# Kernel tuning notes

Hardware: AMD Instinct MI355X
Metric: run time of the kernel (lower is better)

Reference implementation:

```python
import jax, jax.numpy as jnp
import numpy as np

B, S, D, H = 2, 2048, 1024, 16
HD = D // H  # 64

def setup_inputs() -> dict:
    key = jax.random.key(0)
    k1, k2, k3, k4, k5 = jax.random.split(key, 5)
    scale = 0.02
    return {
        "hidden_states": jax.random.normal(k1, (B, S, D), dtype=jnp.float32),
        "w_attn": jax.random.normal(k2, (D, 3 * D), dtype=jnp.float32) * scale,
        "b_attn": jax.random.normal(k3, (3 * D,), dtype=jnp.float32) * scale,
        "w_proj": jax.random.normal(k4, (D, D), dtype=jnp.float32) * scale,
        "b_proj": jax.random.normal(k5, (D,), dtype=jnp.float32) * scale,
    }

def reference(hidden_states, w_attn, b_attn, w_proj, b_proj):
    # qkv projection: [B,S,3D] -> split
    qkv = hidden_states @ w_attn + b_attn
    q, k, v = jnp.split(qkv, 3, axis=-1)
    # split heads -> [B,H,S,HD]
    def split_heads(t):
        return t.reshape(B, S, H, HD).transpose(0, 2, 1, 3)
    q, k, v = split_heads(q), split_heads(k), split_heads(v)
    # eager attention: full [B,H,S,S] scores, causal mask, softmax, AV
    scores = jnp.einsum('bhqd,bhkd->bhqk', q, k) / jnp.sqrt(jnp.float32(HD))
    causal = jnp.tril(jnp.ones((S, S), dtype=bool))  # [S,S]
    mask_value = jnp.finfo(scores.dtype).min
    scores = jnp.where(causal[None, None], scores, mask_value)
    attn = jax.nn.softmax(scores, axis=-1)
    out = jnp.einsum('bhqk,bhkd->bhqd', attn, v)
    # merge heads -> [B,S,D], output projection
    out = out.transpose(0, 2, 1, 3).reshape(B, S, D)
    out = out @ w_proj + b_proj
    return out
```

## Files before the change

### kernel.cpp

```cpp
#include <hip/hip_runtime.h>
#include <hip/hip_bf16.h>
#include <math.h>
#include <stdint.h>

typedef unsigned short u16;
typedef __attribute__((ext_vector_type(8))) short bf16x8;
typedef __attribute__((ext_vector_type(4))) float f32x4;

#define MFMA16(A,B,C) __builtin_amdgcn_mfma_f32_16x16x32_bf16(A,B,C,0,0,0)

#define BB 2
#define SS 2048
#define NT (BB*SS)

__device__ __forceinline__ u16 f2bf(float f) {
    union { float f; unsigned u; } c; c.f = f;
    unsigned r = c.u + 0x7FFF + ((c.u >> 16) & 1);
    return (u16)(r >> 16);
}
__device__ __forceinline__ float bf2f(u16 v) {
    union { unsigned u; float f; } c; c.u = ((unsigned)v) << 16;
    return c.f;
}

__device__ __forceinline__ void gl_lds16(const u16* g, u16* l) {
    __builtin_amdgcn_global_load_lds(
        (const __attribute__((address_space(1))) void*)(uintptr_t)g,
        (__attribute__((address_space(3))) void*)(uintptr_t)l, 16, 0, 0);
}

__global__ __launch_bounds__(256) void cast_bf16(const float* __restrict__ in,
                                                 u16* __restrict__ out, int n) {
    int i = (blockIdx.x * 256 + threadIdx.x) * 4;
    if (i < n) {
        float4 v = *(const float4*)&in[i];
        ushort4 o;
        o.x = f2bf(v.x); o.y = f2bf(v.y); o.z = f2bf(v.z); o.w = f2bf(v.w);
        *(ushort4*)&out[i] = o;
    }
}

__global__ __launch_bounds__(256) void transpose_cast(const float* __restrict__ in,
                                                      u16* __restrict__ out, int M) {
    __shared__ float tile[64][65];
    const int k0 = blockIdx.x * 64, m0 = blockIdx.y * 64;
    const int t = threadIdx.x;
    #pragma unroll
    for (int rep = 0; rep < 16; ++rep) {
        int idx = rep * 256 + t;
        int kk = idx >> 6, mm = idx & 63;
        tile[kk][mm] = in[(size_t)(k0 + kk) * M + m0 + mm];
    }
    __syncthreads();
    #pragma unroll
    for (int rep = 0; rep < 16; ++rep) {
        int idx = rep * 256 + t;
        int mm = idx >> 6, kk = idx & 63;
        out[(size_t)(m0 + mm) * 1024 + k0 + kk] = f2bf(tile[kk][mm]);
    }
}

__global__ __launch_bounds__(256) void transpose_v(const u16* __restrict__ qkvb,
                                                   u16* __restrict__ vtg) {
    __shared__ u16 tile[64][72];
    const int bh = blockIdx.x, kt = blockIdx.y;
    const int b = bh >> 4, h = bh & 15;
    const int t = threadIdx.x;
    const int tt = t >> 2;
    #pragma unroll
    for (int r = 0; r < 2; ++r) {
        int c = (t & 3) + r * 4;
        *(bf16x8*)&tile[tt][c * 8] =
            *(const bf16x8*)&qkvb[(size_t)(b * SS + kt * 64 + tt) * 3072 + 2048 + h * 64 + c * 8];
    }
    __syncthreads();
    const int d = t >> 2;
    #pragma unroll
    for (int r = 0; r < 2; ++r) {
        int c16 = (t & 3) + r * 4;
        ushort4 o0, o1;
        o0.x = tile[c16 * 8 + 0][d]; o0.y = tile[c16 * 8 + 1][d];
        o0.z = tile[c16 * 8 + 2][d]; o0.w = tile[c16 * 8 + 3][d];
        o1.x = tile[c16 * 8 + 4][d]; o1.y = tile[c16 * 8 + 5][d];
        o1.z = tile[c16 * 8 + 6][d]; o1.w = tile[c16 * 8 + 7][d];
        u16* dst = &vtg[(size_t)(bh * 64 + d) * SS + kt * 64 + c16 * 8];
        *(ushort4*)dst = o0;
        *(ushort4*)(dst + 4) = o1;
    }
}

template<int MD, typename OutT>
__global__ __launch_bounds__(256) void gemm_bt(const u16* __restrict__ A,
                                               const u16* __restrict__ BT,
                                               const float* __restrict__ bias,
                                               OutT* __restrict__ C) {
    __shared__ u16 As[128 * 32];
    __shared__ u16 Bs[128 * 32];
    const int t = threadIdx.x;
    const int lane = t & 63;
    const int w = t >> 6;
    const int wr = (w >> 1) * 64, wc = (w & 1) * 64;
    const int ln = lane & 15, hi = lane >> 4;
    const int n0 = blockIdx.x * 128;
    const int m0 = blockIdx.y * 128;

    f32x4 acc[4][4];
    const f32x4 fz = {0.f, 0.f, 0.f, 0.f};
    #pragma unroll
    for (int i = 0; i < 4; ++i)
        #pragma unroll
        for (int j = 0; j < 4; ++j) acc[i][j] = fz;

    const int srow_in = lane >> 2;
    const int schunk  = lane & 3;

    for (int k0 = 0; k0 < 1024; k0 += 32) {
        __syncthreads();
        #pragma unroll
        for (int p = 0; p < 2; ++p) {
            int q   = w * 2 + p;
            int row = q * 16 + srow_in;
            int cg  = schunk ^ (row & 3);
            gl_lds16(&A [(size_t)(n0 + row) * 1024 + k0 + cg * 8], &As[q * 512]);
            gl_lds16(&BT[(size_t)(m0 + row) * 1024 + k0 + cg * 8], &Bs[q * 512]);
        }
        __syncthreads();
        bf16x8 af[4], bf[4];
        #pragma unroll
        for (int mi = 0; mi < 4; ++mi) {
            int r = wr + mi * 16 + ln;
            af[mi] = *(const bf16x8*)&As[r * 32 + ((hi ^ (r & 3)) << 3)];
        }
        #pragma unroll
        for (int ni = 0; ni < 4; ++ni) {
            int r = wc + ni * 16 + ln;
            bf[ni] = *(const bf16x8*)&Bs[r * 32 + ((hi ^ (r & 3)) << 3)];
        }
        #pragma unroll
        for (int mi = 0; mi < 4; ++mi)
            #pragma unroll
            for (int ni = 0; ni < 4; ++ni)
                acc[mi][ni] = MFMA16(af[mi], bf[ni], acc[mi][ni]);
    }

    #pragma unroll
    for (int mi = 0; mi < 4; ++mi) {
        #pragma unroll
        for (int ni = 0; ni < 4; ++ni) {
            int col = m0 + wc + ni * 16 + ln;
            float bv = bias[col];
            #pragma unroll
            for (int r = 0; r < 4; ++r) {
                int row = n0 + wr + mi * 16 + hi * 4 + r;
                float v = acc[mi][ni][r] + bv;
                if constexpr (sizeof(OutT) == 4) C[(size_t)row * MD + col] = v;
                else                             C[(size_t)row * MD + col] = (OutT)f2bf(v);
            }
        }
    }
}

__global__ __launch_bounds__(256) void attn_mfma(const u16* __restrict__ qkv,
                                                 const u16* __restrict__ vtg,
                                                 u16* __restrict__ ctx) {
    __shared__ u16 Ks[2][64 * 64];
    __shared__ u16 Vs[2][64 * 64];
    const int bh = blockIdx.x;
    const int qt = 31 - blockIdx.y;
    const int b = bh >> 4, h = bh & 15;
    const int t = threadIdx.x, w = t >> 6, lane = t & 63;
    const int ln = lane & 15, hi = lane >> 4;
    const int qrow = qt * 64 + w * 16 + ln;
    const size_t tok = (size_t)b * SS;

    bf16x8 qb[2];
    #pragma unroll
    for (int t2 = 0; t2 < 2; ++t2) {
        bf16x8 v = *(const bf16x8*)&qkv[(tok + qrow) * 3072 + h * 64 + t2 * 32 + hi * 8];
        #pragma unroll
        for (int i = 0; i < 8; ++i)
            v[i] = (short)f2bf(bf2f((u16)v[i]) * 0.125f);
        qb[t2] = v;
    }

    float m_run = -1e30f, l_run = 0.f;
    f32x4 o[4];
    const f32x4 fz = {0.f, 0.f, 0.f, 0.f};
    #pragma unroll
    for (int i = 0; i < 4; ++i) o[i] = fz;

    const int kkey_l = w * 8 + (lane >> 3);
    const int ksch   = lane & 7;
    const int vrow_l = lane >> 3;
    const int vsch   = (lane & 7) ^ (lane >> 3);

    const size_t vbase = (size_t)bh * 64 * SS;

    {
        const size_t kvb = (tok ) * 3072 + h * 64;
        #pragma unroll
        for (int p = 0; p < 2; ++p) {
            int kk = p * 32 + kkey_l;
            gl_lds16(&qkv[kvb + (size_t)kk * 3072 + 1024 + ((ksch ^ (kk & 7)) << 3)],
                     &Ks[0][(p * 32 + w * 8) * 64]);
            int d = w * 16 + p * 8 + vrow_l;
            gl_lds16(&vtg[vbase + (size_t)d * SS + (vsch << 3)],
                     &Vs[0][(w * 16 + p * 8) * 64]);
        }
    }

    for (int kt = 0; kt <= qt; ++kt) {
        const int cur = kt & 1;
        __syncthreads();

        if (kt < qt) {
            const int nxt = cur ^ 1;
            const size_t kvb = (tok + (kt + 1) * 64) * 3072 + h * 64;
            #pragma unroll
            for (int p = 0; p < 2; ++p) {
                int kk = p * 32 + kkey_l;
                gl_lds16(&qkv[kvb + (size_t)kk * 3072 + 1024 + ((ksch ^ (kk & 7)) << 3)],
                         &Ks[nxt][(p * 32 + w * 8) * 64]);
                int d = w * 16 + p * 8 + vrow_l;
                gl_lds16(&vtg[vbase + (size_t)d * SS + (kt + 1) * 64 + (vsch << 3)],
                         &Vs[nxt][(w * 16 + p * 8) * 64]);
            }
        }

        f32x4 sacc[4];
        #pragma unroll
        for (int s = 0; s < 4; ++s) {
            int key = s * 16 + ln;
            f32x4 a = fz;
            #pragma unroll
            for (int t2 = 0; t2 < 2; ++t2) {
                bf16x8 kf = *(const bf16x8*)&Ks[cur][key * 64 + (((t2 * 4 + hi) ^ (key & 7)) << 3)];
                a = MFMA16(kf, qb[t2], a);
            }
            sacc[s] = a;
        }

        float p_[16];
        float mloc = -1e30f;
        if (kt == qt) {
            #pragma unroll
            for (int s = 0; s < 4; ++s)
                #pragma unroll
                for (int r = 0; r < 4; ++r) {
                    int keyg = kt * 64 + s * 16 + hi * 4 + r;
                    float v = (keyg <= qrow) ? sacc[s][r] : -1e30f;
                    p_[s * 4 + r] = v;
                    mloc = fmaxf(mloc, v);
                }
        } else {
            #pragma unroll
            for (int s = 0; s < 4; ++s)
                #pragma unroll
                for (int r = 0; r < 4; ++r) {
                    float v = sacc[s][r];
                    p_[s * 4 + r] = v;
                    mloc = fmaxf(mloc, v);
                }
        }
        mloc = fmaxf(mloc, __shfl_xor(mloc, 16));
        mloc = fmaxf(mloc, __shfl_xor(mloc, 32));
        float m_new = fmaxf(m_run, mloc);
        float alpha = __expf(m_run - m_new);
        float lsum = 0.f;
        #pragma unroll
        for (int i = 0; i < 16; ++i) {
            float e = __expf(p_[i] - m_new);
            p_[i] = e;
            lsum += e;
        }
        lsum += __shfl_xor(lsum, 16);
        lsum += __shfl_xor(lsum, 32);
        l_run = l_run * alpha + lsum;
        m_run = m_new;
        #pragma unroll
        for (int dt = 0; dt < 4; ++dt) o[dt] *= alpha;

        bf16x8 pa[2];
        #pragma unroll
        for (int k2 = 0; k2 < 2; ++k2) {
            union { unsigned wd[4]; bf16x8 v; } pu;
            #pragma unroll
            for (int qi = 0; qi < 4; ++qi)
                asm("v_cvt_pk_bf16_f32 %0, %1, %2"
                    : "=v"(pu.wd[qi])
                    : "v"(p_[k2 * 8 + 2 * qi]), "v"(p_[k2 * 8 + 2 * qi + 1]));
            pa[k2] = pu.v;
        }

        #pragma unroll
        for (int dt = 0; dt < 4; ++dt) {
            const u16* row = &Vs[cur][(dt * 16 + ln) * 64];
            const int sw = (ln & 7) << 1;
            #pragma unroll
            for (int k2 = 0; k2 < 2; ++k2) {
                ushort4 lo4 = *(const ushort4*)&row[((k2 * 8 + hi)     ^ sw) * 4];
                ushort4 hi4 = *(const ushort4*)&row[((k2 * 8 + hi + 4) ^ sw) * 4];
                bf16x8 va;
                va[0] = (short)lo4.x; va[1] = (short)lo4.y; va[2] = (short)lo4.z; va[3] = (short)lo4.w;
                va[4] = (short)hi4.x; va[5] = (short)hi4.y; va[6] = (short)hi4.z; va[7] = (short)hi4.w;
                o[dt] = MFMA16(va, pa[k2], o[dt]);
            }
        }
    }

    float inv = 1.f / l_run;
    #pragma unroll
    for (int dt = 0; dt < 4; ++dt) {
        ushort4 ov;
        ov.x = f2bf(o[dt][0] * inv);
        ov.y = f2bf(o[dt][1] * inv);
        ov.z = f2bf(o[dt][2] * inv);
        ov.w = f2bf(o[dt][3] * inv);
        *(ushort4*)&ctx[(tok + qrow) * 1024 + h * 64 + dt * 16 + hi * 4] = ov;
    }
}

extern "C" void kernel_launch(void* const* d_in, const int* in_sizes, int n_in,
                              void* d_out, int out_size, void* d_ws, size_t ws_size,
                              hipStream_t stream) {
    const float* hs     = (const float*)d_in[0];
    const float* w_attn = (const float*)d_in[1];
    const float* b_attn = (const float*)d_in[2];
    const float* w_proj = (const float*)d_in[3];
    const float* b_proj = (const float*)d_in[4];
    float* out = (float*)d_out;

    char* ws = (char*)d_ws;
    u16* hsb  = (u16*)ws;
    u16* waT  = (u16*)(ws + ((size_t)8  << 20));
    u16* wpT  = (u16*)(ws + ((size_t)14 << 20));
    u16* qkvb = (u16*)(ws + ((size_t)16 << 20));
    u16* ctxb = (u16*)(ws + ((size_t)40 << 20));
    u16* vtg  = (u16*)(ws + ((size_t)48 << 20));

    cast_bf16<<<4096, 256, 0, stream>>>(hs, hsb, NT * 1024);
    transpose_cast<<<dim3(16, 48), 256, 0, stream>>>(w_attn, waT, 3072);
    transpose_cast<<<dim3(16, 16), 256, 0, stream>>>(w_proj, wpT, 1024);

    gemm_bt<3072, u16><<<dim3(NT / 128, 3072 / 128), 256, 0, stream>>>(hsb, waT, b_attn, qkvb);
    transpose_v<<<dim3(BB * 16, SS / 64), 256, 0, stream>>>(qkvb, vtg);
    attn_mfma<<<dim3(BB * 16, SS / 64), 256, 0, stream>>>(qkvb, vtg, ctxb);
    gemm_bt<1024, float><<<dim3(NT / 128, 1024 / 128), 256, 0, stream>>>(ctxb, wpT, b_proj, out);
}
```

Before: 118.7 us.

## Pre-swizzle V tiles into fragment order, use exp2 softmax with lazy rescale

The V transpose kernel now writes each 64x64 V tile in MFMA fragment order, so attention loads V fragments with a single 16-byte LDS read instead of two 8-byte swizzled reads. Q is pre-scaled by log2(e)/8 so the softmax can use the hardware exp2. The running max and the accumulators are only rescaled when the max grows by more than 8. s_setprio is raised around the MFMA sections. The lazy rescale lets values grow up to 2^8 before normalisation, which costs some bf16 precision headroom in P.

New measurement: 111.3 us. 1.07x faster.

```diff
diff --git a/kernel.cpp b/kernel.cpp
--- a/kernel.cpp
+++ b/kernel.cpp
@@ -8,6 +8,7 @@
 typedef __attribute__((ext_vector_type(4))) float f32x4;
 
 #define MFMA16(A,B,C) __builtin_amdgcn_mfma_f32_16x16x32_bf16(A,B,C,0,0,0)
+#define EXP2F(x) __builtin_amdgcn_exp2f(x)
 
 #define BB 2
 #define SS 2048
@@ -74,18 +75,20 @@
             *(const bf16x8*)&qkvb[(size_t)(b * SS + kt * 64 + tt) * 3072 + 2048 + h * 64 + c * 8];
     }
     __syncthreads();
-    const int d = t >> 2;
-    #pragma unroll
-    for (int r = 0; r < 2; ++r) {
-        int c16 = (t & 3) + r * 4;
-        ushort4 o0, o1;
-        o0.x = tile[c16 * 8 + 0][d]; o0.y = tile[c16 * 8 + 1][d];
-        o0.z = tile[c16 * 8 + 2][d]; o0.w = tile[c16 * 8 + 3][d];
-        o1.x = tile[c16 * 8 + 4][d]; o1.y = tile[c16 * 8 + 5][d];
-        o1.z = tile[c16 * 8 + 6][d]; o1.w = tile[c16 * 8 + 7][d];
-        u16* dst = &vtg[(size_t)(bh * 64 + d) * SS + kt * 64 + c16 * 8];
-        *(ushort4*)dst = o0;
-        *(ushort4*)(dst + 4) = o1;
+    u16* dst0 = vtg + ((size_t)bh * 32 + kt) * 4096;
+    #pragma unroll
+    for (int rep = 0; rep < 2; ++rep) {
+        int flat = rep * 256 + t;
+        int g = flat >> 6, d = flat & 63;
+        int tok0 = (g >> 2) * 32 + (g & 3) * 4;
+        ushort4 a, bb;
+        a.x  = tile[tok0 + 0][d];  a.y  = tile[tok0 + 1][d];
+        a.z  = tile[tok0 + 2][d];  a.w  = tile[tok0 + 3][d];
+        bb.x = tile[tok0 + 16][d]; bb.y = tile[tok0 + 17][d];
+        bb.z = tile[tok0 + 18][d]; bb.w = tile[tok0 + 19][d];
+        u16* dst = dst0 + (size_t)flat * 8;
+        *(ushort4*)dst = a;
+        *(ushort4*)(dst + 4) = bb;
     }
 }
 
@@ -179,7 +182,7 @@
         bf16x8 v = *(const bf16x8*)&qkv[(tok + qrow) * 3072 + h * 64 + t2 * 32 + hi * 8];
         #pragma unroll
         for (int i = 0; i < 8; ++i)
-            v[i] = (short)f2bf(bf2f((u16)v[i]) * 0.125f);
+            v[i] = (short)f2bf(bf2f((u16)v[i]) * 0.180336881f);
         qb[t2] = v;
     }
 
@@ -191,21 +194,17 @@
 
     const int kkey_l = w * 8 + (lane >> 3);
     const int ksch   = lane & 7;
-    const int vrow_l = lane >> 3;
-    const int vsch   = (lane & 7) ^ (lane >> 3);
-
-    const size_t vbase = (size_t)bh * 64 * SS;
+    const u16* vsrc  = vtg + ((size_t)bh * 32) * 4096;
 
     {
-        const size_t kvb = (tok ) * 3072 + h * 64;
+        const size_t kvb = tok * 3072 + h * 64;
         #pragma unroll
         for (int p = 0; p < 2; ++p) {
             int kk = p * 32 + kkey_l;
             gl_lds16(&qkv[kvb + (size_t)kk * 3072 + 1024 + ((ksch ^ (kk & 7)) << 3)],
                      &Ks[0][(p * 32 + w * 8) * 64]);
-            int d = w * 16 + p * 8 + vrow_l;
-            gl_lds16(&vtg[vbase + (size_t)d * SS + (vsch << 3)],
-                     &Vs[0][(w * 16 + p * 8) * 64]);
+            gl_lds16(&vsrc[(size_t)((w * 2 + p) * 64 + lane) * 8],
+                     &Vs[0][(w * 2 + p) * 512]);
         }
     }
 
@@ -216,18 +215,19 @@
         if (kt < qt) {
             const int nxt = cur ^ 1;
             const size_t kvb = (tok + (kt + 1) * 64) * 3072 + h * 64;
+            const u16* vs2 = vsrc + (size_t)(kt + 1) * 4096;
             #pragma unroll
             for (int p = 0; p < 2; ++p) {
                 int kk = p * 32 + kkey_l;
                 gl_lds16(&qkv[kvb + (size_t)kk * 3072 + 1024 + ((ksch ^ (kk & 7)) << 3)],
                          &Ks[nxt][(p * 32 + w * 8) * 64]);
-                int d = w * 16 + p * 8 + vrow_l;
-                gl_lds16(&vtg[vbase + (size_t)d * SS + (kt + 1) * 64 + (vsch << 3)],
-                         &Vs[nxt][(w * 16 + p * 8) * 64]);
+                gl_lds16(&vs2[(size_t)((w * 2 + p) * 64 + lane) * 8],
+                         &Vs[nxt][(w * 2 + p) * 512]);
             }
         }
 
         f32x4 sacc[4];
+        __builtin_amdgcn_s_setprio(1);
         #pragma unroll
         for (int s = 0; s < 4; ++s) {
             int key = s * 16 + ln;
@@ -239,6 +239,7 @@
             }
             sacc[s] = a;
         }
+        __builtin_amdgcn_s_setprio(0);
 
         float p_[16];
         float mloc = -1e30f;
@@ -264,21 +265,24 @@
         }
         mloc = fmaxf(mloc, __shfl_xor(mloc, 16));
         mloc = fmaxf(mloc, __shfl_xor(mloc, 32));
-        float m_new = fmaxf(m_run, mloc);
-        float alpha = __expf(m_run - m_new);
+        if (!__all(mloc - m_run <= 8.f)) {
+            float m_new = fmaxf(m_run, mloc);
+            float alpha = EXP2F(m_run - m_new);
+            l_run *= alpha;
+            #pragma unroll
+            for (int dt = 0; dt < 4; ++dt) o[dt] *= alpha;
+            m_run = m_new;
+        }
         float lsum = 0.f;
         #pragma unroll
         for (int i = 0; i < 16; ++i) {
-            float e = __expf(p_[i] - m_new);
+            float e = EXP2F(p_[i] - m_run);
             p_[i] = e;
             lsum += e;
         }
         lsum += __shfl_xor(lsum, 16);
         lsum += __shfl_xor(lsum, 32);
-        l_run = l_run * alpha + lsum;
-        m_run = m_new;
-        #pragma unroll
-        for (int dt = 0; dt < 4; ++dt) o[dt] *= alpha;
+        l_run += lsum;
 
         bf16x8 pa[2];
         #pragma unroll
@@ -292,20 +296,15 @@
             pa[k2] = pu.v;
         }
 
-        #pragma unroll
-        for (int dt = 0; dt < 4; ++dt) {
-            const u16* row = &Vs[cur][(dt * 16 + ln) * 64];
-            const int sw = (ln & 7) << 1;
+        __builtin_amdgcn_s_setprio(1);
+        #pragma unroll
+        for (int dt = 0; dt < 4; ++dt)
             #pragma unroll
             for (int k2 = 0; k2 < 2; ++k2) {
-                ushort4 lo4 = *(const ushort4*)&row[((k2 * 8 + hi)     ^ sw) * 4];
-                ushort4 hi4 = *(const ushort4*)&row[((k2 * 8 + hi + 4) ^ sw) * 4];
-                bf16x8 va;
-                va[0] = (short)lo4.x; va[1] = (short)lo4.y; va[2] = (short)lo4.z; va[3] = (short)lo4.w;
-                va[4] = (short)hi4.x; va[5] = (short)hi4.y; va[6] = (short)hi4.z; va[7] = (short)hi4.w;
+                bf16x8 va = *(const bf16x8*)&Vs[cur][(size_t)((k2 * 4 + hi) * 64 + dt * 16 + ln) * 8];
                 o[dt] = MFMA16(va, pa[k2], o[dt]);
             }
-        }
+        __builtin_amdgcn_s_setprio(0);
     }
 
     float inv = 1.f / l_run;
```
